# Kernel optimization log

Measured on AMD Instinct MI355X. Metric: run time of the kernel, lower is better.

Reference implementation:

```python
import jax, jax.numpy as jnp
import numpy as np

N = 50000   # nodes
E = 800000  # edges (avg degree 16)
G = 256     # graphs in batch
IN = 64; H = 128; K = 8; C = 10; L = 3
TAU = 1.0


def _bn(x, g, b, eps=1e-5):
    # BatchNorm1d training-mode forward: batch stats over the row dim.
    m = x.mean(0)
    v = x.var(0)
    return (x - m) * jax.lax.rsqrt(v + eps) * g + b


def _ln(x, g, b, eps=1e-5):
    m = x.mean(-1, keepdims=True)
    v = x.var(-1, keepdims=True)
    return (x - m) * jax.lax.rsqrt(v + eps) * g + b


def setup_inputs() -> dict:
    key = jax.random.key(0)
    ks = jax.random.split(key, 16)
    p = lambda k, shape: jax.random.normal(k, shape, jnp.float32) * 0.05
    u = jax.random.uniform(ks[2], (N, K), minval=1e-10, maxval=1.0)
    return {
        "x": jax.random.normal(ks[0], (N, IN), jnp.float32),
        "edge_index": jax.random.randint(ks[1], (2, E), 0, N, dtype=jnp.int32),
        "batch": (jnp.arange(N, dtype=jnp.int32) * G) // N,  # sorted, all graphs present
        "gumbel": -jnp.log(-jnp.log(u)),  # fixed Gumbel(0,1) noise
        "inp_w": p(ks[3], (IN, H)), "inp_b": jnp.zeros(H),
        "elin_w": p(ks[4], (L, 1, H)), "elin_b": jnp.zeros((L, H)),
        "mlp1_w": p(ks[5], (L, H, H)), "mlp1_b": jnp.zeros((L, H)),
        "mlpbn_g": jnp.ones((L, H)), "mlpbn_b": jnp.zeros((L, H)),
        "mlp2_w": p(ks[6], (L, H, H)), "mlp2_b": jnp.zeros((L, H)),
        "bn_g": jnp.ones((L, H)), "bn_b": jnp.zeros((L, H)),
        "bh1_w": p(ks[7], (H, H // 2)), "bh1_b": jnp.zeros(H // 2),
        "bh2_w": p(ks[8], (H // 2, K)), "bh2_b": jnp.zeros(K),
        "bm_w": p(ks[9], (H, H)), "bm_b": jnp.zeros(H),
        "ln_g": jnp.ones(H), "ln_b": jnp.zeros(H),
        "clf1_w": p(ks[10], (2 * H, H)), "clf1_b": jnp.zeros(H),
        "clfbn_g": jnp.ones(H), "clfbn_b": jnp.zeros(H),
        "clf2_w": p(ks[11], (H, C)), "clf2_b": jnp.zeros(C),
    }


def reference(x, edge_index, batch, gumbel, inp_w, inp_b, elin_w, elin_b,
              mlp1_w, mlp1_b, mlpbn_g, mlpbn_b, mlp2_w, mlp2_b, bn_g, bn_b,
              bh1_w, bh1_b, bh2_w, bh2_b, bm_w, bm_b, ln_g, ln_b,
              clf1_w, clf1_b, clfbn_g, clfbn_b, clf2_w, clf2_b):
    src, dst = edge_index[0], edge_index[1]
    h = x @ inp_w + inp_b  # [N,H]
    for l in range(L):  # GINEConv stack (eps=0, dummy edge attr = ones[E,1])
        e_emb = elin_w[l][0] + elin_b[l]          # ones @ W + b -> single [H] vector
        msg = jax.nn.relu(h[src] + e_emb)          # gather + add, [E,H]
        aggr = jax.ops.segment_sum(msg, dst, num_segments=N)  # scatter-add
        z = h + aggr                               # (1+eps)*x + aggr, eps=0
        z = jax.nn.relu(_bn(z @ mlp1_w[l] + mlp1_b[l], mlpbn_g[l], mlpbn_b[l]))
        z = z @ mlp2_w[l] + mlp2_b[l]
        h = jax.nn.relu(_bn(z, bn_g[l], bn_b[l]))
    # blob assignment via gumbel-softmax (soft)
    logits = jax.nn.relu(h @ bh1_w + bh1_b) @ bh2_w + bh2_b  # [N,K]
    assign = jax.nn.softmax((logits + gumbel) / TAU, axis=-1)
    counts = jax.ops.segment_sum(jnp.ones((N,), h.dtype), batch, num_segments=G)
    gmean = jax.ops.segment_sum(h, batch, num_segments=G) / counts[:, None]  # [G,H]
    # per-graph weighted blob pooling, vectorized over graphs via segment_sum
    num = jax.ops.segment_sum(assign[:, :, None] * h[:, None, :], batch, num_segments=G)  # [G,K,H]
    den = jax.ops.segment_sum(assign, batch, num_segments=G)  # [G,K]
    blobs = num / (den[:, :, None] + 1e-8)
    blobs = _ln(jax.nn.relu(blobs @ bm_w + bm_b), ln_g, ln_b)
    blob_emb = blobs.max(axis=1)  # [G,H]
    z = jnp.concatenate([gmean, blob_emb], axis=-1)  # [G,2H]
    z = jax.nn.relu(_bn(z @ clf1_w + clf1_b, clfbn_g, clfbn_b))
    return z @ clf2_w + clf2_b  # [G,C]
```

## Files before the change

### kernel.cpp

```cpp
#include <hip/hip_runtime.h>
#include <hip/hip_bf16.h>


#define HH 128
typedef unsigned short u16;
typedef unsigned int u32;
typedef __attribute__((ext_vector_type(8))) short bf16x8;
typedef __attribute__((ext_vector_type(4))) float f32x4;

__device__ __forceinline__ void atomAddF(float* p, float v) { unsafeAtomicAdd(p, v); }

__device__ __forceinline__ u16 f2bf(float f) {
    u32 u = __float_as_uint(f);
    u += 0x7fffu + ((u >> 16) & 1u);
    return (u16)(u >> 16);
}
__device__ __forceinline__ float bf2f_lo(u32 u) { return __uint_as_float(u << 16); }
__device__ __forceinline__ float bf2f_hi(u32 u) { return __uint_as_float(u & 0xffff0000u); }
__device__ __forceinline__ void split2(float v, u16& hi, u16& lo) {
    u16 h_ = f2bf(v);
    float hf = __uint_as_float(((u32)h_) << 16);
    hi = h_;
    lo = f2bf(v - hf);
}
__device__ __forceinline__ u32 swz(u32 row, u32 kByte, u32 strideB) {
    return (row * strideB + kByte) ^ ((row & 7u) << 4);
}

#define WTOT (8192 + 6 * 16384)

__global__ void k_prep(const float* __restrict__ inp_w, const float* __restrict__ m1,
                       const float* __restrict__ m2, u16* __restrict__ Whi,
                       u16* __restrict__ Wlo) {
    int b = blockIdx.x;
    int t = threadIdx.x;
    if (b == 0) {
        for (int idx = t; idx < 128 * 64; idx += 256) {
            int c = idx >> 6, k = idx & 63;
            u16 hi, lo;
            split2(inp_w[k * 128 + c], hi, lo);
            Whi[idx] = hi; Wlo[idx] = lo;
        }
    } else {
        const float* W = (b <= 3) ? m1 + (size_t)(b - 1) * 16384
                                  : m2 + (size_t)(b - 4) * 16384;
        u16* dh = Whi + 8192 + (size_t)(b - 1) * 16384;
        u16* dl = Wlo + 8192 + (size_t)(b - 1) * 16384;
        for (int idx = t; idx < 16384; idx += 256) {
            int c = idx >> 7, k = idx & 127;
            u16 hi, lo;
            split2(W[k * 128 + c], hi, lo);
            dh[idx] = hi; dl[idx] = lo;
        }
    }
}

__global__ void k_hist(const int* __restrict__ ei, int* __restrict__ deg, int E) {
    int i4 = blockIdx.x * 256 + threadIdx.x;
    int e0 = i4 * 4;
    if (e0 + 3 < E) {
        int4 d = *(const int4*)(ei + E + e0);
        atomicAdd(&deg[d.x], 1);
        atomicAdd(&deg[d.y], 1);
        atomicAdd(&deg[d.z], 1);
        atomicAdd(&deg[d.w], 1);
    } else {
        for (int e = e0; e < E; e++) atomicAdd(&deg[ei[E + e]], 1);
    }
}

__global__ void k_bsum(const int* __restrict__ deg, int* __restrict__ bsum, int N) {
    int t = threadIdx.x;
    int i = blockIdx.x * 256 + t;
    int v = (i < N) ? deg[i] : 0;
    for (int o = 32; o; o >>= 1) v += __shfl_down(v, o);
    __shared__ int ws_[4];
    if ((t & 63) == 0) ws_[t >> 6] = v;
    __syncthreads();
    if (t == 0) bsum[blockIdx.x] = ws_[0] + ws_[1] + ws_[2] + ws_[3];
}

__global__ void k_scan1(const int* __restrict__ bsum, int* __restrict__ boff,
                        int* __restrict__ rowptrN, int nch) {
    int t = threadIdx.x;
    int v = (t < nch) ? bsum[t] : 0;
    int l = t & 63, w = t >> 6;
    int sv = v;
    for (int o = 1; o < 64; o <<= 1) { int u = __shfl_up(sv, o); if (l >= o) sv += u; }
    __shared__ int wsum[4];
    if (l == 63) wsum[w] = sv;
    __syncthreads();
    int add = 0;
    for (int j = 0; j < w; j++) add += wsum[j];
    if (t < nch) boff[t] = sv - v + add;
    if (t == nch - 1) *rowptrN = sv + add;
}

__global__ void k_scan2(const int* __restrict__ deg, const int* __restrict__ boff,
                        int* __restrict__ rowptr, int* __restrict__ cursor, int N) {
    int b = blockIdx.x, t = threadIdx.x, i = b * 256 + t;
    int v = (i < N) ? deg[i] : 0;
    int l = t & 63, w = t >> 6;
    int sv = v;
    for (int o = 1; o < 64; o <<= 1) { int u = __shfl_up(sv, o); if (l >= o) sv += u; }
    __shared__ int wsum[4];
    if (l == 63) wsum[w] = sv;
    __syncthreads();
    int add = boff[b];
    for (int j = 0; j < w; j++) add += wsum[j];
    if (i < N) { int e = sv - v + add; rowptr[i] = e; cursor[i] = e; }
}

__global__ void k_fill(const int* __restrict__ ei, int* __restrict__ cursor,
                       int* __restrict__ col, int E) {
    int i4 = blockIdx.x * 256 + threadIdx.x;
    int e0 = i4 * 4;
    if (e0 + 3 < E) {
        int4 s = *(const int4*)(ei + e0);
        int4 d = *(const int4*)(ei + E + e0);
        int p0 = atomicAdd(&cursor[d.x], 1);
        int p1 = atomicAdd(&cursor[d.y], 1);
        int p2 = atomicAdd(&cursor[d.z], 1);
        int p3 = atomicAdd(&cursor[d.w], 1);
        col[p0] = s.x;
        col[p1] = s.y;
        col[p2] = s.z;
        col[p3] = s.w;
    } else {
        for (int e = e0; e < E; e++) {
            int pos = atomicAdd(&cursor[ei[E + e]], 1);
            col[pos] = ei[e];
        }
    }
}

template <int KD, int MODE, bool STATS, bool FOUT, bool BOUT>
__global__ __launch_bounds__(512) void k_mgemm(
    const float* __restrict__ inf, const u16* __restrict__ inhi,
    const u16* __restrict__ inlo, const u16* __restrict__ Whi,
    const u16* __restrict__ Wlo, const float* __restrict__ bias,
    const float* __restrict__ statsIn, const float* __restrict__ gamma,
    const float* __restrict__ beta, float invN,
    float* __restrict__ out, u16* __restrict__ outb,
    float* __restrict__ statsOut, int Nrows, int ntiles) {
    __shared__ u16 s_Ahi[128 * KD];
    __shared__ u16 s_Alo[128 * KD];
    __shared__ u16 s_Bhi[128 * KD];
    __shared__ u16 s_Blo[128 * KD];
    __shared__ float s_red[2][8][128];
    __shared__ float s_sc[128], s_sh[128];
    const int t = threadIdx.x;
    constexpr u32 STR = KD * 2;
    constexpr int KCB = KD / 8;
    constexpr int KCF = KD / 4;
    constexpr int NAU = (128 * KCB) / 512;
    constexpr int NAF = (128 * KCF) / 512;
    constexpr int NB  = (128 * KCB) / 512;

#pragma unroll
    for (int i = 0; i < NB; i++) {
        int idx = i * 512 + t;
        int c = idx / KCB, kc = idx % KCB;
        u32 off = swz(c, kc * 16, STR);
        *(uint4*)((char*)s_Bhi + off) = *(const uint4*)(Whi + (size_t)c * KD + kc * 8);
        *(uint4*)((char*)s_Blo + off) = *(const uint4*)(Wlo + (size_t)c * KD + kc * 8);
    }
    if (MODE == 1 && t < 128) {
        float m = statsIn[t] * invN;
        float var = statsIn[128 + t] * invN - m * m;
        float s = gamma[t] * rsqrtf(var + 1e-5f);
        s_sc[t] = s;
        s_sh[t] = beta[t] - m * s;
    }
    __syncthreads();

    float4 rf[MODE <= 1 ? NAF : 1];
    uint4 rh[MODE == 2 ? NAU : 1], rl[MODE == 2 ? NAU : 1];
    int tile = blockIdx.x;
    if (tile < ntiles) {
        if (MODE <= 1) {
#pragma unroll
            for (int i = 0; i < NAF; i++) {
                int idx = i * 512 + t;
                int r = idx / KCF, kc = idx % KCF;
                int gr = tile * 128 + r;
                rf[i] = (gr < Nrows) ? *(const float4*)(inf + (size_t)gr * KD + kc * 4)
                                     : (float4){0.f, 0.f, 0.f, 0.f};
            }
        } else {
#pragma unroll
            for (int i = 0; i < NAU; i++) {
                int idx = i * 512 + t;
                int r = idx / KCB, kc = idx % KCB;
                int gr = tile * 128 + r;
                if (gr < Nrows) {
                    rh[i] = *(const uint4*)(inhi + (size_t)gr * KD + kc * 8);
                    rl[i] = *(const uint4*)(inlo + (size_t)gr * KD + kc * 8);
                } else {
                    rh[i] = (uint4){0, 0, 0, 0};
                    rl[i] = (uint4){0, 0, 0, 0};
                }
            }
        }
    }

    const int l = t & 63, w = t >> 6;
    const int c0 = l & 15;
    const u32 kOffB = (u32)(l >> 4) * 16u;
    const u32 rA_row = w * 16 + c0;

    for (; tile < ntiles; tile += gridDim.x) {
        if (MODE <= 1) {
#pragma unroll
            for (int i = 0; i < NAF; i++) {
                int idx = i * 512 + t;
                int r = idx / KCF, kc = idx % KCF;
                float4 v = rf[i];
                if (MODE == 1) {
                    int k0 = kc * 4;
                    v.x = fmaxf(v.x * s_sc[k0 + 0] + s_sh[k0 + 0], 0.f);
                    v.y = fmaxf(v.y * s_sc[k0 + 1] + s_sh[k0 + 1], 0.f);
                    v.z = fmaxf(v.z * s_sc[k0 + 2] + s_sh[k0 + 2], 0.f);
                    v.w = fmaxf(v.w * s_sc[k0 + 3] + s_sh[k0 + 3], 0.f);
                }
                u16 h0, h1, h2, h3, l0, l1, l2, l3;
                split2(v.x, h0, l0); split2(v.y, h1, l1);
                split2(v.z, h2, l2); split2(v.w, h3, l3);
                uint2 ph = {(u32)h0 | ((u32)h1 << 16), (u32)h2 | ((u32)h3 << 16)};
                uint2 pl = {(u32)l0 | ((u32)l1 << 16), (u32)l2 | ((u32)l3 << 16)};
                u32 off = swz(r, kc * 8, STR);
                *(uint2*)((char*)s_Ahi + off) = ph;
                *(uint2*)((char*)s_Alo + off) = pl;
            }
        } else {
#pragma unroll
            for (int i = 0; i < NAU; i++) {
                int idx = i * 512 + t;
                int r = idx / KCB, kc = idx % KCB;
                u32 off = swz(r, kc * 16, STR);
                *(uint4*)((char*)s_Ahi + off) = rh[i];
                *(uint4*)((char*)s_Alo + off) = rl[i];
            }
        }
        __syncthreads();

        int nxt = tile + gridDim.x;
        if (nxt < ntiles) {
            if (MODE <= 1) {
#pragma unroll
                for (int i = 0; i < NAF; i++) {
                    int idx = i * 512 + t;
                    int r = idx / KCF, kc = idx % KCF;
                    int gr = nxt * 128 + r;
                    rf[i] = (gr < Nrows) ? *(const float4*)(inf + (size_t)gr * KD + kc * 4)
                                         : (float4){0.f, 0.f, 0.f, 0.f};
                }
            } else {
#pragma unroll
                for (int i = 0; i < NAU; i++) {
                    int idx = i * 512 + t;
                    int r = idx / KCB, kc = idx % KCB;
                    int gr = nxt * 128 + r;
                    if (gr < Nrows) {
                        rh[i] = *(const uint4*)(inhi + (size_t)gr * KD + kc * 8);
                        rl[i] = *(const uint4*)(inlo + (size_t)gr * KD + kc * 8);
                    } else {
                        rh[i] = (uint4){0, 0, 0, 0};
                        rl[i] = (uint4){0, 0, 0, 0};
                    }
                }
            }
        }

        f32x4 acc[8];
#pragma unroll
        for (int n = 0; n < 8; n++) acc[n] = (f32x4){0.f, 0.f, 0.f, 0.f};
#pragma unroll
        for (int kk = 0; kk < KD / 32; kk++) {
            u32 kb = kk * 64 + kOffB;
            bf16x8 ah = *(const bf16x8*)((char*)s_Ahi + swz(rA_row, kb, STR));
            bf16x8 al = *(const bf16x8*)((char*)s_Alo + swz(rA_row, kb, STR));
#pragma unroll
            for (int n = 0; n < 8; n++) {
                u32 ob = swz(n * 16 + c0, kb, STR);
                bf16x8 bh = *(const bf16x8*)((char*)s_Bhi + ob);
                bf16x8 bl = *(const bf16x8*)((char*)s_Blo + ob);
                acc[n] = __builtin_amdgcn_mfma_f32_16x16x32_bf16(ah, bh, acc[n], 0, 0, 0);
                acc[n] = __builtin_amdgcn_mfma_f32_16x16x32_bf16(al, bh, acc[n], 0, 0, 0);
                acc[n] = __builtin_amdgcn_mfma_f32_16x16x32_bf16(ah, bl, acc[n], 0, 0, 0);
            }
        }

        const int rbase = tile * 128 + w * 16 + ((l >> 4) << 2);
#pragma unroll
        for (int n = 0; n < 8; n++) {
            const int colc = n * 16 + c0;
            const float bv = bias[colc];
            float s = 0.f, q = 0.f;
#pragma unroll
            for (int j = 0; j < 4; j++) {
                int gr = rbase + j;
                if (gr < Nrows) {
                    float v = acc[n][j] + bv;
                    if (FOUT) out[(size_t)gr * HH + colc] = v;
                    if (BOUT) outb[(size_t)gr * HH + colc] = f2bf(v);
                    s += v;
                    q += v * v;
                }
            }
            if (STATS) {
                s += __shfl_xor(s, 16); s += __shfl_xor(s, 32);
                q += __shfl_xor(q, 16); q += __shfl_xor(q, 32);
                if (l < 16) {
                    s_red[0][w][n * 16 + l] = s;
                    s_red[1][w][n * 16 + l] = q;
                }
            }
        }
        __syncthreads();
        if (STATS && t < 128) {
            float S = 0.f, Q = 0.f;
#pragma unroll
            for (int ww = 0; ww < 8; ww++) { S += s_red[0][ww][t]; Q += s_red[1][ww][t]; }
            atomAddF(&statsOut[t], S);
            atomAddF(&statsOut[HH + t], Q);
        }
    }
}

__global__ __launch_bounds__(256) void k_gather(
    const u16* __restrict__ hb,
    const int* __restrict__ rowptr, const int* __restrict__ col,
    const float* __restrict__ ew, const float* __restrict__ eb,
    u16* __restrict__ zhi, u16* __restrict__ zlo, int N) {
    __shared__ float2 s_part[2][64];
    const int wv = threadIdx.x >> 6;
    const int lane = threadIdx.x & 63;
    const int node = blockIdx.x * 2 + (wv >> 1);
    const int hf = wv & 1;
    const int c2 = lane * 2;
    float2 acc = {0.f, 0.f};
    const bool valid = node < N;
    float2 ee = {0.f, 0.f};
    if (valid) {
        ee.x = ew[c2] + eb[c2];
        ee.y = ew[c2 + 1] + eb[c2 + 1];
        const int s = rowptr[node], eend = rowptr[node + 1];
        int e = s + hf;
        for (; e + 14 < eend; e += 16) {
            int s0 = col[e], s1 = col[e + 2], s2 = col[e + 4], s3 = col[e + 6];
            int s4 = col[e + 8], s5 = col[e + 10], s6 = col[e + 12], s7 = col[e + 14];
            u32 u0 = *(const u32*)(hb + (size_t)s0 * HH + c2);
            u32 u1 = *(const u32*)(hb + (size_t)s1 * HH + c2);
            u32 u2 = *(const u32*)(hb + (size_t)s2 * HH + c2);
            u32 u3 = *(const u32*)(hb + (size_t)s3 * HH + c2);
            u32 u4 = *(const u32*)(hb + (size_t)s4 * HH + c2);
            u32 u5 = *(const u32*)(hb + (size_t)s5 * HH + c2);
            u32 u6 = *(const u32*)(hb + (size_t)s6 * HH + c2);
            u32 u7 = *(const u32*)(hb + (size_t)s7 * HH + c2);
            acc.x += fmaxf(bf2f_lo(u0) + ee.x, 0.f) + fmaxf(bf2f_lo(u1) + ee.x, 0.f) +
                     fmaxf(bf2f_lo(u2) + ee.x, 0.f) + fmaxf(bf2f_lo(u3) + ee.x, 0.f) +
                     fmaxf(bf2f_lo(u4) + ee.x, 0.f) + fmaxf(bf2f_lo(u5) + ee.x, 0.f) +
                     fmaxf(bf2f_lo(u6) + ee.x, 0.f) + fmaxf(bf2f_lo(u7) + ee.x, 0.f);
            acc.y += fmaxf(bf2f_hi(u0) + ee.y, 0.f) + fmaxf(bf2f_hi(u1) + ee.y, 0.f) +
                     fmaxf(bf2f_hi(u2) + ee.y, 0.f) + fmaxf(bf2f_hi(u3) + ee.y, 0.f) +
                     fmaxf(bf2f_hi(u4) + ee.y, 0.f) + fmaxf(bf2f_hi(u5) + ee.y, 0.f) +
                     fmaxf(bf2f_hi(u6) + ee.y, 0.f) + fmaxf(bf2f_hi(u7) + ee.y, 0.f);
        }
        for (; e + 6 < eend; e += 8) {
            int s0 = col[e], s1 = col[e + 2], s2 = col[e + 4], s3 = col[e + 6];
            u32 u0 = *(const u32*)(hb + (size_t)s0 * HH + c2);
            u32 u1 = *(const u32*)(hb + (size_t)s1 * HH + c2);
            u32 u2 = *(const u32*)(hb + (size_t)s2 * HH + c2);
            u32 u3 = *(const u32*)(hb + (size_t)s3 * HH + c2);
            acc.x += fmaxf(bf2f_lo(u0) + ee.x, 0.f) + fmaxf(bf2f_lo(u1) + ee.x, 0.f) +
                     fmaxf(bf2f_lo(u2) + ee.x, 0.f) + fmaxf(bf2f_lo(u3) + ee.x, 0.f);
            acc.y += fmaxf(bf2f_hi(u0) + ee.y, 0.f) + fmaxf(bf2f_hi(u1) + ee.y, 0.f) +
                     fmaxf(bf2f_hi(u2) + ee.y, 0.f) + fmaxf(bf2f_hi(u3) + ee.y, 0.f);
        }
        for (; e < eend; e += 2) {
            u32 u0 = *(const u32*)(hb + (size_t)col[e] * HH + c2);
            acc.x += fmaxf(bf2f_lo(u0) + ee.x, 0.f);
            acc.y += fmaxf(bf2f_hi(u0) + ee.y, 0.f);
        }
    }
    if (hf) s_part[wv >> 1][lane] = acc;
    __syncthreads();
    if (!hf && valid) {
        float2 p = s_part[wv >> 1][lane];
        u32 un = *(const u32*)(hb + (size_t)node * HH + c2);
        float zx = bf2f_lo(un) + acc.x + p.x;
        float zy = bf2f_hi(un) + acc.y + p.y;
        u16 h0, h1, l0, l1;
        split2(zx, h0, l0);
        split2(zy, h1, l1);
        *(u32*)(zhi + (size_t)node * HH + c2) = (u32)h0 | ((u32)h1 << 16);
        *(u32*)(zlo + (size_t)node * HH + c2) = (u32)l0 | ((u32)l1 << 16);
    }
}

template <bool WF>
__global__ void k_bnrelu(const float* __restrict__ t, const float* __restrict__ stats,
                         const float* __restrict__ g, const float* __restrict__ b,
                         float invN, float* __restrict__ h, u16* __restrict__ hb,
                         int total4) {
    int i = blockIdx.x * 256 + threadIdx.x;
    if (i >= total4) return;
    int c4 = (i & 31) << 2;
    float sc[4], sh[4];
#pragma unroll
    for (int j = 0; j < 4; j++) {
        float m = stats[c4 + j] * invN;
        float var = stats[128 + c4 + j] * invN - m * m;
        float s = g[c4 + j] * rsqrtf(var + 1e-5f);
        sc[j] = s;
        sh[j] = b[c4 + j] - m * s;
    }
    float4 v = *(const float4*)(t + (size_t)i * 4);
    float4 o;
    o.x = fmaxf(v.x * sc[0] + sh[0], 0.f);
    o.y = fmaxf(v.y * sc[1] + sh[1], 0.f);
    o.z = fmaxf(v.z * sc[2] + sh[2], 0.f);
    o.w = fmaxf(v.w * sc[3] + sh[3], 0.f);
    if (WF) *(float4*)(h + (size_t)i * 4) = o;
    uint2 p = {(u32)f2bf(o.x) | ((u32)f2bf(o.y) << 16),
               (u32)f2bf(o.z) | ((u32)f2bf(o.w) << 16)};
    *(uint2*)(hb + (size_t)i * 4) = p;
}

__global__ __launch_bounds__(256) void k_assign(
    const float* __restrict__ h, const float* __restrict__ gum,
    const float* __restrict__ w1, const float* __restrict__ b1,
    const float* __restrict__ w2, const float* __restrict__ b2,
    float* __restrict__ assign, int N) {
    __shared__ float s_w1[128 * 64];
    __shared__ float s_w2[64 * 8];
    __shared__ float s_h[32][128];
    __shared__ float s_hid[32][64];
    const int t = threadIdx.x;
    const int n0 = blockIdx.x * 32;
    for (int i = t; i < 128 * 64; i += 256) s_w1[i] = w1[i];
    for (int i = t; i < 512; i += 256) s_w2[i] = w2[i];
    for (int i = t; i < 32 * 32; i += 256) {
        int r = i >> 5, c4 = (i & 31) << 2;
        int gn = n0 + r;
        float4 v = {0.f, 0.f, 0.f, 0.f};
        if (gn < N) v = *(const float4*)(h + (size_t)gn * HH + c4);
        *(float4*)(&s_h[r][c4]) = v;
    }
    __syncthreads();
    for (int o = t; o < 32 * 64; o += 256) {
        int nn = o >> 6, j = o & 63;
        float acc = b1[j];
        for (int k = 0; k < 128; k++) acc = fmaf(s_h[nn][k], s_w1[k * 64 + j], acc);
        s_hid[nn][j] = fmaxf(acc, 0.f);
    }
    __syncthreads();
    int nn = t >> 3, kk = t & 7;
    int gn = n0 + nn;
    float a = b2[kk];
    for (int j = 0; j < 64; j++) a = fmaf(s_hid[nn][j], s_w2[j * 8 + kk], a);
    if (gn < N) a += gum[(size_t)gn * 8 + kk];
    float m = a;
    m = fmaxf(m, __shfl_xor(m, 1));
    m = fmaxf(m, __shfl_xor(m, 2));
    m = fmaxf(m, __shfl_xor(m, 4));
    float e = expf(a - m);
    float s = e;
    s += __shfl_xor(s, 1); s += __shfl_xor(s, 2); s += __shfl_xor(s, 4);
    if (gn < N) assign[(size_t)gn * 8 + kk] = e / s;
}

__device__ __forceinline__ int lowerb(const int* __restrict__ arr, int n, int val) {
    int lo = 0, hi = n;
    while (lo < hi) {
        int mid = (lo + hi) >> 1;
        if (arr[mid] < val) lo = mid + 1;
        else hi = mid;
    }
    return lo;
}

__global__ __launch_bounds__(1024) void k_pool(
    const float* __restrict__ h, const float* __restrict__ assign,
    const int* __restrict__ batch, float* __restrict__ gmean,
    float* __restrict__ num, float* __restrict__ den, int N) {
    __shared__ float4 s_num[4][8][32];
    __shared__ float4 s_gm[4][32];
    __shared__ float s_den[4][8];
    const int g = blockIdx.x;
    const int t = threadIdx.x;
    const int ns = t >> 8;
    const int k = (t >> 5) & 7;
    const int lane = t & 31;
    const int c4 = lane << 2;
    const int start = lowerb(batch, N, g);
    const int end = lowerb(batch, N, g + 1);
    float4 an = {0.f, 0.f, 0.f, 0.f};
    float4 gm = {0.f, 0.f, 0.f, 0.f};
    float ad = 0.f;
    for (int n = start + ns; n < end; n += 4) {
        float a = assign[(size_t)n * 8 + k];
        const float4 hv = *(const float4*)(h + (size_t)n * HH + c4);
        an.x = fmaf(a, hv.x, an.x);
        an.y = fmaf(a, hv.y, an.y);
        an.z = fmaf(a, hv.z, an.z);
        an.w = fmaf(a, hv.w, an.w);
        if (k == 0) { gm.x += hv.x; gm.y += hv.y; gm.z += hv.z; gm.w += hv.w; }
        ad += a;
    }
    s_num[ns][k][lane] = an;
    if (k == 0) s_gm[ns][lane] = gm;
    if (lane == 0) s_den[ns][k] = ad;
    __syncthreads();
    if (t < 256) {
        float4 a0 = s_num[0][k][lane], a1 = s_num[1][k][lane];
        float4 a2 = s_num[2][k][lane], a3 = s_num[3][k][lane];
        float4 o = {a0.x + a1.x + a2.x + a3.x, a0.y + a1.y + a2.y + a3.y,
                    a0.z + a1.z + a2.z + a3.z, a0.w + a1.w + a2.w + a3.w};
        *(float4*)(num + ((size_t)g * 8 + k) * HH + c4) = o;
        if (t < 32) {
            float4 g0 = s_gm[0][lane], g1 = s_gm[1][lane];
            float4 g2 = s_gm[2][lane], g3 = s_gm[3][lane];
            int cnt = end - start;
            float inv = 1.f / (float)(cnt > 0 ? cnt : 1);
            float4 om = {(g0.x + g1.x + g2.x + g3.x) * inv,
                         (g0.y + g1.y + g2.y + g3.y) * inv,
                         (g0.z + g1.z + g2.z + g3.z) * inv,
                         (g0.w + g1.w + g2.w + g3.w) * inv};
            *(float4*)(gmean + (size_t)g * HH + c4) = om;
        }
        if (t < 8) den[(size_t)g * 8 + t] =
            s_den[0][t] + s_den[1][t] + s_den[2][t] + s_den[3][t];
    }
}

__global__ void k_blob(const float* __restrict__ num, const float* __restrict__ den,
                       const float* __restrict__ w, const float* __restrict__ b,
                       const float* __restrict__ lg, const float* __restrict__ lb,
                       float* __restrict__ blobs) {
    const int gk = blockIdx.x;
    const int c = threadIdx.x;
    __shared__ float srow[128];
    __shared__ float red[4];
    float d = den[gk] + 1e-8f;
    srow[c] = num[(size_t)gk * HH + c] / d;
    __syncthreads();
    float acc = b[c];
    for (int j = 0; j < 128; j++) acc = fmaf(srow[j], w[j * HH + c], acc);
    float y = fmaxf(acc, 0.f);
    float s = y, q = y * y;
    for (int off = 32; off > 0; off >>= 1) {
        s += __shfl_down(s, off);
        q += __shfl_down(q, off);
    }
    if ((c & 63) == 0) { red[(c >> 6) * 2] = s; red[(c >> 6) * 2 + 1] = q; }
    __syncthreads();
    float S = red[0] + red[2], Q = red[1] + red[3];
    float m = S * (1.f / 128.f);
    float var = Q * (1.f / 128.f) - m * m;
    blobs[(size_t)gk * HH + c] = (y - m) * rsqrtf(var + 1e-5f) * lg[c] + lb[c];
}

__global__ void k_clf1(const float* __restrict__ gmean, const float* __restrict__ blobs,
                       const float* __restrict__ w, const float* __restrict__ bias,
                       float* __restrict__ t4, float* __restrict__ stats) {
    int g = blockIdx.x;
    int c = threadIdx.x;
    __shared__ float s[256];
    float m = blobs[((size_t)g * 8) * HH + c];
#pragma unroll
    for (int k = 1; k < 8; k++) m = fmaxf(m, blobs[((size_t)g * 8 + k) * HH + c]);
    s[c] = gmean[(size_t)g * HH + c];
    s[128 + c] = m;
    __syncthreads();
    float acc = bias[c];
    for (int j = 0; j < 256; j++) acc = fmaf(s[j], w[j * HH + c], acc);
    t4[(size_t)g * HH + c] = acc;
    atomAddF(&stats[c], acc);
    atomAddF(&stats[HH + c], acc * acc);
}

__global__ void k_clf2(const float* __restrict__ t4, const float* __restrict__ stats,
                       const float* __restrict__ g_, const float* __restrict__ b_,
                       float invG, const float* __restrict__ w,
                       const float* __restrict__ bias, float* __restrict__ out) {
    int g = blockIdx.x;
    int t = threadIdx.x;
    __shared__ float s[128];
    float m = stats[t] * invG;
    float var = stats[128 + t] * invG - m * m;
    float sc = g_[t] * rsqrtf(var + 1e-5f);
    float sh = b_[t] - m * sc;
    s[t] = fmaxf(t4[(size_t)g * HH + t] * sc + sh, 0.f);
    __syncthreads();
    if (t < 10) {
        float acc = bias[t];
        for (int j = 0; j < 128; j++) acc = fmaf(s[j], w[j * 10 + t], acc);
        out[(size_t)g * 10 + t] = acc;
    }
}

extern "C" void kernel_launch(void* const* d_in, const int* in_sizes, int n_in,
                              void* d_out, int out_size, void* d_ws, size_t ws_size,
                              hipStream_t stream) {
    const float* x      = (const float*)d_in[0];
    const int*   ei     = (const int*)d_in[1];
    const int*   batch  = (const int*)d_in[2];
    const float* gumbel = (const float*)d_in[3];
    const float* inp_w  = (const float*)d_in[4];
    const float* inp_b  = (const float*)d_in[5];
    const float* elin_w = (const float*)d_in[6];
    const float* elin_b = (const float*)d_in[7];
    const float* mlp1_w = (const float*)d_in[8];
    const float* mlp1_b = (const float*)d_in[9];
    const float* mlpbn_g = (const float*)d_in[10];
    const float* mlpbn_b = (const float*)d_in[11];
    const float* mlp2_w = (const float*)d_in[12];
    const float* mlp2_b = (const float*)d_in[13];
    const float* bn_g   = (const float*)d_in[14];
    const float* bn_b   = (const float*)d_in[15];
    const float* bh1_w  = (const float*)d_in[16];
    const float* bh1_b  = (const float*)d_in[17];
    const float* bh2_w  = (const float*)d_in[18];
    const float* bh2_b  = (const float*)d_in[19];
    const float* bm_w   = (const float*)d_in[20];
    const float* bm_b   = (const float*)d_in[21];
    const float* ln_g   = (const float*)d_in[22];
    const float* ln_b   = (const float*)d_in[23];
    const float* clf1_w = (const float*)d_in[24];
    const float* clf1_b = (const float*)d_in[25];
    const float* clfbn_g = (const float*)d_in[26];
    const float* clfbn_b = (const float*)d_in[27];
    const float* clf2_w = (const float*)d_in[28];
    const float* clf2_b = (const float*)d_in[29];
    float* out = (float*)d_out;

    const int N = in_sizes[0] / 64;
    const int E = in_sizes[1] / 2;
    const int G = out_size / 10;

    float* ws = (float*)d_ws;
    float* h      = ws;
    float* zbuf   = h + (size_t)N * HH;
    float* t1     = zbuf + (size_t)N * HH;
    float* assign = t1 + (size_t)N * HH;
    float* gmean  = assign + (size_t)N * 8;
    float* num    = gmean + (size_t)G * HH;
    float* den    = num + (size_t)G * 8 * HH;
    float* blobs  = den + (size_t)G * 8;
    float* t4     = blobs + (size_t)G * 8 * HH;
    float* statsA = t4 + (size_t)G * HH;
    u16* Whi = (u16*)(statsA + 7 * 256);
    u16* Wlo = Whi + WTOT;
    int* rowptr = (int*)(Wlo + WTOT);
    int* cursor = rowptr + (N + 1);
    int* colidx = cursor + N;
    int* bsum   = colidx + E;
    int* boff   = bsum + 256;
    u16* hb  = (u16*)t1;
    u16* zhi = (u16*)zbuf;
    u16* zlo = zhi + (size_t)N * HH;
    float* t2 = zbuf;

    const dim3 B256(256), B128(128), B512(512), B1024(1024);
    const int ntiles = (N + 127) / 128;
    const int gg = ntiles < 256 ? ntiles : 256;
    const int nch = (N + 255) / 256;
    const int e4 = (E + 4 * 256 - 1) / (4 * 256);
    const float invN = 1.f / (float)N;
    const float invG = 1.f / (float)G;

    k_prep<<<7, B256, 0, stream>>>(inp_w, mlp1_w, mlp2_w, Whi, Wlo);
    hipMemsetAsync(cursor, 0, (size_t)N * sizeof(int), stream);
    hipMemsetAsync(statsA, 0, 7 * 256 * sizeof(float), stream);
    k_hist<<<e4, B256, 0, stream>>>(ei, cursor, E);
    k_bsum<<<nch, B256, 0, stream>>>(cursor, bsum, N);
    k_scan1<<<1, B256, 0, stream>>>(bsum, boff, rowptr + N, nch);
    k_scan2<<<nch, B256, 0, stream>>>(cursor, boff, rowptr, cursor, N);
    k_fill<<<e4, B256, 0, stream>>>(ei, cursor, colidx, E);

    k_mgemm<64, 0, false, false, true><<<gg, B512, 0, stream>>>(
        x, nullptr, nullptr, Whi, Wlo, inp_b, nullptr, nullptr, nullptr, 0.f,
        nullptr, hb, nullptr, N, ntiles);

    for (int l = 0; l < 3; l++) {
        float* sa = statsA + (size_t)(2 * l) * 256;
        float* sb = statsA + (size_t)(2 * l + 1) * 256;
        k_gather<<<(N + 1) / 2, B256, 0, stream>>>(hb, rowptr, colidx,
                                                   elin_w + l * HH, elin_b + l * HH,
                                                   zhi, zlo, N);
        k_mgemm<128, 2, true, true, false><<<gg, B512, 0, stream>>>(
            nullptr, zhi, zlo, Whi + 8192 + (size_t)l * 16384,
            Wlo + 8192 + (size_t)l * 16384, mlp1_b + l * HH,
            nullptr, nullptr, nullptr, 0.f, t1, nullptr, sa, N, ntiles);
        k_mgemm<128, 1, true, true, false><<<gg, B512, 0, stream>>>(
            t1, nullptr, nullptr, Whi + 8192 + (size_t)(3 + l) * 16384,
            Wlo + 8192 + (size_t)(3 + l) * 16384, mlp2_b + l * HH,
            sa, mlpbn_g + l * HH, mlpbn_b + l * HH, invN, t2, nullptr, sb, N, ntiles);
        if (l < 2)
            k_bnrelu<false><<<(N * 32 + 255) / 256, B256, 0, stream>>>(
                t2, sb, bn_g + l * HH, bn_b + l * HH, invN, nullptr, hb, N * 32);
        else
            k_bnrelu<true><<<(N * 32 + 255) / 256, B256, 0, stream>>>(
                t2, sb, bn_g + l * HH, bn_b + l * HH, invN, h, hb, N * 32);
    }

    k_assign<<<(N + 31) / 32, B256, 0, stream>>>(h, gumbel, bh1_w, bh1_b, bh2_w, bh2_b, assign, N);
    k_pool<<<G, B1024, 0, stream>>>(h, assign, batch, gmean, num, den, N);
    k_blob<<<G * 8, B128, 0, stream>>>(num, den, bm_w, bm_b, ln_g, ln_b, blobs);
    float* sc_ = statsA + 6 * 256;
    k_clf1<<<G, B128, 0, stream>>>(gmean, blobs, clf1_w, clf1_b, t4, sc_);
    k_clf2<<<G, B128, 0, stream>>>(t4, sc_, clfbn_g, clfbn_b, invG, clf2_w, clf2_b, out);
}
```

Measured before the change: 508.6 us.

## Load GEMM A fragments directly from global into registers, drop LDS staging

The row-tile GEMM no longer stages the A operand through shared memory. Each lane now loads its own MFMA fragment rows straight from global memory, applying the optional BN+ReLU and the hi/lo bf16 split in registers. This removes the A-tile LDS writes and reads plus one barrier per tile, and the grid size rises from 256 to 512 blocks to add parallelism because the LDS footprint is smaller. In exchange it drops the register prefetch of the next tile, so global loads are no longer overlapped with compute. Each lane's loads are also less coalesced, with strided 16-byte reads per row. A barrier is added after the stats reduction to protect s_red reuse.

```diff
diff --git a/kernel.cpp b/kernel.cpp
--- a/kernel.cpp
+++ b/kernel.cpp
@@ -143,8 +143,6 @@
     const float* __restrict__ beta, float invN,
     float* __restrict__ out, u16* __restrict__ outb,
     float* __restrict__ statsOut, int Nrows, int ntiles) {
-    __shared__ u16 s_Ahi[128 * KD];
-    __shared__ u16 s_Alo[128 * KD];
     __shared__ u16 s_Bhi[128 * KD];
     __shared__ u16 s_Blo[128 * KD];
     __shared__ float s_red[2][8][128];
@@ -152,10 +150,8 @@
     const int t = threadIdx.x;
     constexpr u32 STR = KD * 2;
     constexpr int KCB = KD / 8;
-    constexpr int KCF = KD / 4;
-    constexpr int NAU = (128 * KCB) / 512;
-    constexpr int NAF = (128 * KCF) / 512;
-    constexpr int NB  = (128 * KCB) / 512;
+    constexpr int NB = (128 * KCB) / 512;
+    constexpr int NF = KD / 32;
 
 #pragma unroll
     for (int i = 0; i < NB; i++) {
@@ -174,120 +170,74 @@
     }
     __syncthreads();
 
-    float4 rf[MODE <= 1 ? NAF : 1];
-    uint4 rh[MODE == 2 ? NAU : 1], rl[MODE == 2 ? NAU : 1];
-    int tile = blockIdx.x;
-    if (tile < ntiles) {
-        if (MODE <= 1) {
-#pragma unroll
-            for (int i = 0; i < NAF; i++) {
-                int idx = i * 512 + t;
-                int r = idx / KCF, kc = idx % KCF;
-                int gr = tile * 128 + r;
-                rf[i] = (gr < Nrows) ? *(const float4*)(inf + (size_t)gr * KD + kc * 4)
-                                     : (float4){0.f, 0.f, 0.f, 0.f};
+    const int l = t & 63, w = t >> 6;
+    const int c0 = l & 15;
+    const int ksub = (l >> 4) * 8;
+    const u32 kOffB = (u32)(l >> 4) * 16u;
+
+    for (int tile = blockIdx.x; tile < ntiles; tile += gridDim.x) {
+        const int row = tile * 128 + w * 16 + c0;
+        const bool rv = row < Nrows;
+
+        bf16x8 ah[NF], al[NF];
+        if (MODE == 2) {
+#pragma unroll
+            for (int kk = 0; kk < NF; kk++) {
+                int k0 = kk * 32 + ksub;
+                if (rv) {
+                    ah[kk] = *(const bf16x8*)(inhi + (size_t)row * KD + k0);
+                    al[kk] = *(const bf16x8*)(inlo + (size_t)row * KD + k0);
+                } else {
+                    uint4 z = {0, 0, 0, 0};
+                    ah[kk] = *(bf16x8*)&z;
+                    al[kk] = *(bf16x8*)&z;
+                }
             }
         } else {
 #pragma unroll
-            for (int i = 0; i < NAU; i++) {
-                int idx = i * 512 + t;
-                int r = idx / KCB, kc = idx % KCB;
-                int gr = tile * 128 + r;
-                if (gr < Nrows) {
-                    rh[i] = *(const uint4*)(inhi + (size_t)gr * KD + kc * 8);
-                    rl[i] = *(const uint4*)(inlo + (size_t)gr * KD + kc * 8);
-                } else {
-                    rh[i] = (uint4){0, 0, 0, 0};
-                    rl[i] = (uint4){0, 0, 0, 0};
+            for (int kk = 0; kk < NF; kk++) {
+                int k0 = kk * 32 + ksub;
+                float4 v0 = {0.f, 0.f, 0.f, 0.f}, v1 = {0.f, 0.f, 0.f, 0.f};
+                if (rv) {
+                    v0 = *(const float4*)(inf + (size_t)row * KD + k0);
+                    v1 = *(const float4*)(inf + (size_t)row * KD + k0 + 4);
                 }
+                float vv[8] = {v0.x, v0.y, v0.z, v0.w, v1.x, v1.y, v1.z, v1.w};
+                uint4 uh, ul;
+                u32* ph = (u32*)&uh;
+                u32* pl = (u32*)&ul;
+#pragma unroll
+                for (int p = 0; p < 4; p++) {
+                    float a0 = vv[2 * p], a1 = vv[2 * p + 1];
+                    if (MODE == 1) {
+                        a0 = fmaxf(a0 * s_sc[k0 + 2 * p] + s_sh[k0 + 2 * p], 0.f);
+                        a1 = fmaxf(a1 * s_sc[k0 + 2 * p + 1] + s_sh[k0 + 2 * p + 1], 0.f);
+                    }
+                    u16 h0, l0, h1, l1;
+                    split2(a0, h0, l0);
+                    split2(a1, h1, l1);
+                    ph[p] = (u32)h0 | ((u32)h1 << 16);
+                    pl[p] = (u32)l0 | ((u32)l1 << 16);
+                }
+                ah[kk] = *(bf16x8*)&uh;
+                al[kk] = *(bf16x8*)&ul;
             }
         }
-    }
-
-    const int l = t & 63, w = t >> 6;
-    const int c0 = l & 15;
-    const u32 kOffB = (u32)(l >> 4) * 16u;
-    const u32 rA_row = w * 16 + c0;
-
-    for (; tile < ntiles; tile += gridDim.x) {
-        if (MODE <= 1) {
-#pragma unroll
-            for (int i = 0; i < NAF; i++) {
-                int idx = i * 512 + t;
-                int r = idx / KCF, kc = idx % KCF;
-                float4 v = rf[i];
-                if (MODE == 1) {
-                    int k0 = kc * 4;
-                    v.x = fmaxf(v.x * s_sc[k0 + 0] + s_sh[k0 + 0], 0.f);
-                    v.y = fmaxf(v.y * s_sc[k0 + 1] + s_sh[k0 + 1], 0.f);
-                    v.z = fmaxf(v.z * s_sc[k0 + 2] + s_sh[k0 + 2], 0.f);
-                    v.w = fmaxf(v.w * s_sc[k0 + 3] + s_sh[k0 + 3], 0.f);
-                }
-                u16 h0, h1, h2, h3, l0, l1, l2, l3;
-                split2(v.x, h0, l0); split2(v.y, h1, l1);
-                split2(v.z, h2, l2); split2(v.w, h3, l3);
-                uint2 ph = {(u32)h0 | ((u32)h1 << 16), (u32)h2 | ((u32)h3 << 16)};
-                uint2 pl = {(u32)l0 | ((u32)l1 << 16), (u32)l2 | ((u32)l3 << 16)};
-                u32 off = swz(r, kc * 8, STR);
-                *(uint2*)((char*)s_Ahi + off) = ph;
-                *(uint2*)((char*)s_Alo + off) = pl;
-            }
-        } else {
-#pragma unroll
-            for (int i = 0; i < NAU; i++) {
-                int idx = i * 512 + t;
-                int r = idx / KCB, kc = idx % KCB;
-                u32 off = swz(r, kc * 16, STR);
-                *(uint4*)((char*)s_Ahi + off) = rh[i];
-                *(uint4*)((char*)s_Alo + off) = rl[i];
-            }
-        }
-        __syncthreads();
-
-        int nxt = tile + gridDim.x;
-        if (nxt < ntiles) {
-            if (MODE <= 1) {
-#pragma unroll
-                for (int i = 0; i < NAF; i++) {
-                    int idx = i * 512 + t;
-                    int r = idx / KCF, kc = idx % KCF;
-                    int gr = nxt * 128 + r;
-                    rf[i] = (gr < Nrows) ? *(const float4*)(inf + (size_t)gr * KD + kc * 4)
-                                         : (float4){0.f, 0.f, 0.f, 0.f};
-                }
-            } else {
-#pragma unroll
-                for (int i = 0; i < NAU; i++) {
-                    int idx = i * 512 + t;
-                    int r = idx / KCB, kc = idx % KCB;
-                    int gr = nxt * 128 + r;
-                    if (gr < Nrows) {
-                        rh[i] = *(const uint4*)(inhi + (size_t)gr * KD + kc * 8);
-                        rl[i] = *(const uint4*)(inlo + (size_t)gr * KD + kc * 8);
-                    } else {
-                        rh[i] = (uint4){0, 0, 0, 0};
-                        rl[i] = (uint4){0, 0, 0, 0};
-                    }
-                }
-            }
-        }
 
         f32x4 acc[8];
 #pragma unroll
         for (int n = 0; n < 8; n++) acc[n] = (f32x4){0.f, 0.f, 0.f, 0.f};
 #pragma unroll
-        for (int kk = 0; kk < KD / 32; kk++) {
+        for (int kk = 0; kk < NF; kk++) {
             u32 kb = kk * 64 + kOffB;
-            bf16x8 ah = *(const bf16x8*)((char*)s_Ahi + swz(rA_row, kb, STR));
-            bf16x8 al = *(const bf16x8*)((char*)s_Alo + swz(rA_row, kb, STR));
 #pragma unroll
             for (int n = 0; n < 8; n++) {
                 u32 ob = swz(n * 16 + c0, kb, STR);
                 bf16x8 bh = *(const bf16x8*)((char*)s_Bhi + ob);
                 bf16x8 bl = *(const bf16x8*)((char*)s_Blo + ob);
-                acc[n] = __builtin_amdgcn_mfma_f32_16x16x32_bf16(ah, bh, acc[n], 0, 0, 0);
-                acc[n] = __builtin_amdgcn_mfma_f32_16x16x32_bf16(al, bh, acc[n], 0, 0, 0);
-                acc[n] = __builtin_amdgcn_mfma_f32_16x16x32_bf16(ah, bl, acc[n], 0, 0, 0);
+                acc[n] = __builtin_amdgcn_mfma_f32_16x16x32_bf16(ah[kk], bh, acc[n], 0, 0, 0);
+                acc[n] = __builtin_amdgcn_mfma_f32_16x16x32_bf16(al[kk], bh, acc[n], 0, 0, 0);
+                acc[n] = __builtin_amdgcn_mfma_f32_16x16x32_bf16(ah[kk], bl, acc[n], 0, 0, 0);
             }
         }
 
@@ -317,13 +267,16 @@
                 }
             }
         }
-        __syncthreads();
-        if (STATS && t < 128) {
-            float S = 0.f, Q = 0.f;
-#pragma unroll
-            for (int ww = 0; ww < 8; ww++) { S += s_red[0][ww][t]; Q += s_red[1][ww][t]; }
-            atomAddF(&statsOut[t], S);
-            atomAddF(&statsOut[HH + t], Q);
+        if (STATS) {
+            __syncthreads();
+            if (t < 128) {
+                float S = 0.f, Q = 0.f;
+#pragma unroll
+                for (int ww = 0; ww < 8; ww++) { S += s_red[0][ww][t]; Q += s_red[1][ww][t]; }
+                atomAddF(&statsOut[t], S);
+                atomAddF(&statsOut[HH + t], Q);
+            }
+            __syncthreads();
         }
     }
 }
@@ -665,7 +618,7 @@
 
     const dim3 B256(256), B128(128), B512(512), B1024(1024);
     const int ntiles = (N + 127) / 128;
-    const int gg = ntiles < 256 ? ntiles : 256;
+    const int gg = ntiles < 512 ? ntiles : 512;
     const int nch = (N + 255) / 256;
     const int e4 = (E + 4 * 256 - 1) / (4 * 256);
     const float invN = 1.f / (float)N;
```

Measured after the change: 511.2 us. Within noise of the previous version (+0.5%).
